# Optimization experiments

Measured on AMD Instinct MI355X. Metric: run time of the kernel, lower is better.

The kernel has to match this reference:

```python
import jax, jax.numpy as jnp
import numpy as np

B, H, S, D = 2, 16, 2048, 64
MASK_P = 0.1  # sparse random mask; avoids all-heads-masked NaN under softmax(dim=1)


def setup_inputs() -> dict:
    key = jax.random.key(0)
    kq, kk, kv, km = jax.random.split(key, 4)
    Q = jax.random.normal(kq, (B, H, S, D), dtype=jnp.float32)
    K = jax.random.normal(kk, (B, H, S, D), dtype=jnp.float32)
    V = jax.random.normal(kv, (B, H, S, D), dtype=jnp.float32)
    mask_bool = jax.random.uniform(km, (B, H, S, S)) < MASK_P
    return {"Q": Q, "K": K, "V": V, "mask_bool": mask_bool, "head_dim": D}


def reference(Q, K, V, mask_bool, head_dim):
    scale = jnp.sqrt(jnp.asarray(head_dim, dtype=Q.dtype))
    # scores: [B, H, Sq, Sk]
    scores = jnp.einsum("bhqd,bhkd->bhqk", Q, K) / scale
    scores = jnp.where(mask_bool, -jnp.inf, scores)
    # NOTE: source uses torch.softmax(..., dim=1) -> normalize over HEADS axis.
    attention_weight = jax.nn.softmax(scores, axis=1)
    # dropout module treated as identity (eval mode)
    context = jnp.einsum("bhqk,bhkd->bhqd", attention_weight, V)
    # transpose(1, 2) -> [B, Sq, H, D]
    return jnp.transpose(context, (0, 2, 1, 3))
```

## Files before the change

kernel.cpp:

```cpp
#include <hip/hip_runtime.h>
#include <stdint.h>
#include <math.h>

#define BB 2
#define HH 16
#define SS 2048
#define DD 64
#define QE  ((size_t)BB * HH * SS * DD)
#define PME ((size_t)BB * SS * SS)

typedef __attribute__((ext_vector_type(8))) short short8;
typedef __attribute__((ext_vector_type(4))) float float4v;

__device__ __forceinline__ float bflo(unsigned int u){ return __uint_as_float(u << 16); }
__device__ __forceinline__ float bfhi(unsigned int u){ return __uint_as_float(u & 0xffff0000u); }
__device__ __forceinline__ unsigned short f2bf(float f){
  unsigned int u = __float_as_uint(f);
  u += 0x7fffu + ((u >> 16) & 1u);
  return (unsigned short)(u >> 16);
}
__device__ __forceinline__ unsigned int pk2(float lo, float hi){
  return ((unsigned int)f2bf(hi) << 16) | (unsigned int)f2bf(lo);
}

__global__ void detect_mask_mode(const unsigned int* __restrict__ mw, int* __restrict__ mode_out){
  __shared__ int a32, af, a64;
  const int t = threadIdx.x;
  if (t == 0){ a32 = 1; af = 1; a64 = 1; }
  __syncthreads();
  int ok32 = 1, okf = 1, ok64 = 1;
  for (int idx = t; idx < 4096; idx += 256){
    const unsigned int w = mw[idx];
    if (w > 1u) ok32 = 0;
    if (w != 0u && w != 0x3F800000u) okf = 0;
    if ((idx & 1) ? (w != 0u) : (w > 1u)) ok64 = 0;
  }
  if (!ok32) atomicAnd(&a32, 0);
  if (!okf)  atomicAnd(&af, 0);
  if (!ok64) atomicAnd(&a64, 0);
  __syncthreads();
  if (t == 0){
    int mode;
    if (a64)      mode = 3;
    else if (a32) mode = 0;
    else if (af)  mode = 2;
    else          mode = 1;
    *mode_out = mode;
  }
}

__global__ __launch_bounds__(256) void pack_mask_kernel(
    const void* __restrict__ mask, const int* __restrict__ modep,
    unsigned short* __restrict__ pm)
{
  const int mode = *modep;
  const size_t tid  = (size_t)blockIdx.x * 256 + threadIdx.x;
  const size_t base = tid * 8;
  const size_t bq   = base >> 11;
  const int    k0   = (int)(base & (SS - 1));
  const size_t b    = bq >> 11;
  const size_t q    = bq & (SS - 1);

  unsigned short outv[8] = {0,0,0,0,0,0,0,0};

  if (mode == 0 || mode == 2){
    const unsigned int* p = (const unsigned int*)mask;
    #pragma unroll
    for (int h = 0; h < HH; ++h){
      const size_t e = ((b * HH + h) * SS + q) * SS + k0;
      const uint4 a = *(const uint4*)(p + e);
      const uint4 c = *(const uint4*)(p + e + 4);
      const unsigned short bit = (unsigned short)(1u << h);
      if (a.x) outv[0] |= bit;  if (a.y) outv[1] |= bit;
      if (a.z) outv[2] |= bit;  if (a.w) outv[3] |= bit;
      if (c.x) outv[4] |= bit;  if (c.y) outv[5] |= bit;
      if (c.z) outv[6] |= bit;  if (c.w) outv[7] |= bit;
    }
  } else if (mode == 1){
    const unsigned char* p = (const unsigned char*)mask;
    #pragma unroll
    for (int h = 0; h < HH; ++h){
      const size_t e = ((b * HH + h) * SS + q) * SS + k0;
      uint2 a = *(const uint2*)(p + e);
      const unsigned short bit = (unsigned short)(1u << h);
      #pragma unroll
      for (int j = 0; j < 4; ++j){
        if ((a.x >> (8*j)) & 0xffu) outv[j]     |= bit;
        if ((a.y >> (8*j)) & 0xffu) outv[4 + j] |= bit;
      }
    }
  } else {
    const unsigned int* p = (const unsigned int*)mask;
    #pragma unroll
    for (int h = 0; h < HH; ++h){
      const size_t e = (((b * HH + h) * SS + q) * SS + k0) * 2;
      const unsigned short bit = (unsigned short)(1u << h);
      #pragma unroll
      for (int j = 0; j < 4; ++j){
        const uint4 a = *(const uint4*)(p + e + j * 4);
        if (a.x) outv[j * 2]     |= bit;
        if (a.z) outv[j * 2 + 1] |= bit;
      }
    }
  }

  uint4 w;
  w.x = (unsigned int)outv[0] | ((unsigned int)outv[1] << 16);
  w.y = (unsigned int)outv[2] | ((unsigned int)outv[3] << 16);
  w.z = (unsigned int)outv[4] | ((unsigned int)outv[5] << 16);
  w.w = (unsigned int)outv[6] | ((unsigned int)outv[7] << 16);
  *(uint4*)(pm + base) = w;
}

__global__ void conv_bf16_kernel(const float* __restrict__ src, unsigned short* __restrict__ dst, float scale){
  const size_t i = ((size_t)blockIdx.x * 256 + threadIdx.x) * 8;
  const float4 a = *(const float4*)(src + i);
  const float4 b = *(const float4*)(src + i + 4);
  uint4 o;
  o.x = pk2(a.x * scale, a.y * scale);
  o.y = pk2(a.z * scale, a.w * scale);
  o.z = pk2(b.x * scale, b.y * scale);
  o.w = pk2(b.z * scale, b.w * scale);
  *(uint4*)(dst + i) = o;
}

__global__ void transp_v_kernel(const float* __restrict__ V, unsigned short* __restrict__ Vt){
  __shared__ unsigned short tile[64][66];
  const int t  = threadIdx.x;
  const int kt = blockIdx.x & 31;
  const int bh = blockIdx.x >> 5;
  {
    const int kr = t >> 2, dc = (t & 3) * 16;
    const float* src = V + ((size_t)bh * SS + (size_t)(kt * 64 + kr)) * DD + dc;
    #pragma unroll
    for (int c = 0; c < 4; ++c){
      const float4 v = *(const float4*)(src + c * 4);
      tile[kr][dc + c * 4 + 0] = f2bf(v.x);
      tile[kr][dc + c * 4 + 1] = f2bf(v.y);
      tile[kr][dc + c * 4 + 2] = f2bf(v.z);
      tile[kr][dc + c * 4 + 3] = f2bf(v.w);
    }
  }
  __syncthreads();
  {
    const int dr = t >> 2, kc = (t & 3) * 16;
    unsigned short* dst = Vt + ((size_t)bh * DD + dr) * SS + kt * 64 + kc;
    unsigned int w[8];
    #pragma unroll
    for (int p = 0; p < 8; ++p){
      w[p] = (unsigned int)tile[kc + 2*p][dr] | ((unsigned int)tile[kc + 2*p + 1][dr] << 16);
    }
    uint4 o0 = { w[0], w[1], w[2], w[3] };
    uint4 o1 = { w[4], w[5], w[6], w[7] };
    *(uint4*)(dst)     = o0;
    *(uint4*)(dst + 8) = o1;
  }
}

__global__ __launch_bounds__(256, 2) void attn_main_kernel(
    const unsigned short* __restrict__ Qb, const unsigned short* __restrict__ Kb,
    const unsigned short* __restrict__ Vt, const unsigned short* __restrict__ pm,
    float* __restrict__ out)
{
  __shared__ unsigned short Qf[HH * 2 * 512];
  __shared__ unsigned short W[HH * 16 * 64];

  const int t = threadIdx.x;
  const int wave = t >> 6, lane = t & 63, quad = lane >> 4, l16 = lane & 15;

  const int L  = blockIdx.x;
  const int b  = (L >> 1) & 1;
  const int kc = (L >> 2) & 1;
  const int q0 = (((L >> 3) << 1) | (L & 1)) * 16;

  float4v O[4][4];
  #pragma unroll
  for (int i = 0; i < 4; ++i)
    #pragma unroll
    for (int j = 0; j < 4; ++j) O[i][j] = (float4v){0.f, 0.f, 0.f, 0.f};

  #pragma unroll
  for (int hh = 0; hh < 4; ++hh){
    const int h = wave * 4 + hh;
    const unsigned short* qp = Qb + ((size_t)(b * HH + h) * SS + (size_t)(q0 + l16)) * DD + quad * 8;
    const short8 a0 = *(const short8*)(qp);
    const short8 a1 = *(const short8*)(qp + 32);
    *(short8*)&Qf[(h * 2 + 0) * 512 + lane * 8] = a0;
    *(short8*)&Qf[(h * 2 + 1) * 512 + lane * 8] = a1;
  }
  __syncthreads();

  #pragma unroll 1
  for (int ks = 0; ks < 16; ++ks){
    const int k0  = (kc * 16 + ks) * 64;
    const int k0w = k0 + wave * 16;

    const unsigned short* pmb = pm + ((size_t)b * SS + (size_t)(q0 + quad * 4)) * SS + (size_t)(k0w + l16);
    unsigned int m16[4];
    #pragma unroll
    for (int r = 0; r < 4; ++r) m16[r] = (unsigned int)pmb[(size_t)r * SS];

    unsigned int sp[HH][2];
    const unsigned short* kbase = Kb + ((size_t)(b * HH) * SS + (size_t)(k0w + l16)) * DD + quad * 8;

    #pragma unroll
    for (int ch = 0; ch < 2; ++ch){
      short8 kb0[8], kb1[8];
      #pragma unroll
      for (int j = 0; j < 8; ++j){
        const unsigned short* kp = kbase + (size_t)(ch * 8 + j) * (SS * DD);
        kb0[j] = *(const short8*)(kp);
        kb1[j] = *(const short8*)(kp + 32);
      }
      #pragma unroll
      for (int j = 0; j < 8; ++j){
        const int h = ch * 8 + j;
        const short8 a0 = *(const short8*)&Qf[(h * 2 + 0) * 512 + lane * 8];
        const short8 a1 = *(const short8*)&Qf[(h * 2 + 1) * 512 + lane * 8];
        float4v c = (float4v){0.f, 0.f, 0.f, 0.f};
        c = __builtin_amdgcn_mfma_f32_16x16x32_bf16(a0, kb0[j], c, 0, 0, 0);
        c = __builtin_amdgcn_mfma_f32_16x16x32_bf16(a1, kb1[j], c, 0, 0, 0);
        #pragma unroll
        for (int r = 0; r < 4; ++r) if ((m16[r] >> h) & 1u) c[r] = -INFINITY;
        sp[h][0] = pk2(c[0], c[1]);
        sp[h][1] = pk2(c[2], c[3]);
      }
    }

    #pragma unroll
    for (int r = 0; r < 4; ++r){
      const int row = quad * 4 + r;
      float sv[HH];
      float m = -INFINITY;
      #pragma unroll
      for (int h = 0; h < HH; ++h){
        const unsigned int u = sp[h][r >> 1];
        const float f = (r & 1) ? bfhi(u) : bflo(u);
        sv[h] = f;
        m = fmaxf(m, f);
      }
      float sum = 0.f;
      #pragma unroll
      for (int h = 0; h < HH; ++h){
        const float e = (sv[h] != -INFINITY) ? __expf(sv[h] - m) : 0.f;
        sv[h] = e;
        sum += e;
      }
      const float rinv = (sum > 0.f) ? (1.0f / sum) : 0.f;
      const int col = (wave * 16 + l16) ^ ((row & 7) << 3);
      #pragma unroll
      for (int h = 0; h < HH; ++h){
        W[h * 1024 + row * 64 + col] = f2bf(sv[h] * rinv);
      }
    }
    __syncthreads();

    {
      short8 aw[8];
      #pragma unroll
      for (int hh = 0; hh < 4; ++hh)
        #pragma unroll
        for (int kr = 0; kr < 2; ++kr){
          const int h = wave * 4 + hh;
          aw[hh * 2 + kr] = *(const short8*)&W[h * 1024 + l16 * 64 + ((kr * 32 + quad * 8) ^ ((l16 & 7) << 3))];
        }

      short8 vb[2][8];
      {
        const unsigned short* v0 = Vt + ((size_t)(b * HH + wave * 4) * DD + l16) * SS + k0 + quad * 8;
        #pragma unroll
        for (int kr = 0; kr < 2; ++kr)
          #pragma unroll
          for (int dt = 0; dt < 4; ++dt)
            vb[0][kr * 4 + dt] = *(const short8*)(v0 + (size_t)dt * 16 * SS + kr * 32);
      }
      #pragma unroll
      for (int hh = 0; hh < 4; ++hh){
        const int cur = hh & 1;
        if (hh < 3){
          const unsigned short* v1 = Vt + ((size_t)(b * HH + wave * 4 + hh + 1) * DD + l16) * SS + k0 + quad * 8;
          #pragma unroll
          for (int kr = 0; kr < 2; ++kr)
            #pragma unroll
            for (int dt = 0; dt < 4; ++dt)
              vb[cur ^ 1][kr * 4 + dt] = *(const short8*)(v1 + (size_t)dt * 16 * SS + kr * 32);
        }
        #pragma unroll
        for (int kr = 0; kr < 2; ++kr)
          #pragma unroll
          for (int dt = 0; dt < 4; ++dt)
            O[hh][dt] = __builtin_amdgcn_mfma_f32_16x16x32_bf16(aw[hh * 2 + kr], vb[cur][kr * 4 + dt], O[hh][dt], 0, 0, 0);
      }
    }
    __syncthreads();
  }

  #pragma unroll
  for (int hh = 0; hh < 4; ++hh){
    const int h = wave * 4 + hh;
    #pragma unroll
    for (int dt = 0; dt < 4; ++dt){
      #pragma unroll
      for (int r = 0; r < 4; ++r){
        float* op = out + (((size_t)b * SS + (size_t)(q0 + quad * 4 + r)) * HH + h) * DD + dt * 16 + l16;
        unsafeAtomicAdd(op, O[hh][dt][r]);
      }
    }
  }
}

extern "C" void kernel_launch(void* const* d_in, const int* in_sizes, int n_in,
                              void* d_out, int out_size, void* d_ws, size_t ws_size,
                              hipStream_t stream)
{
  const float* Q = (const float*)d_in[0];
  const float* K = (const float*)d_in[1];
  const float* V = (const float*)d_in[2];
  const void* mask = d_in[3];

  uintptr_t base = (uintptr_t)d_ws;
  int* mode_ptr       = (int*)base;
  unsigned short* Qb  = (unsigned short*)(base + 64);
  unsigned short* Kb  = Qb + QE;
  unsigned short* Vt  = Kb + QE;
  unsigned short* pmp = Vt + QE;

  detect_mask_mode<<<1, 256, 0, stream>>>((const unsigned int*)mask, mode_ptr);
  pack_mask_kernel<<<(int)(PME / (256 * 8)), 256, 0, stream>>>(mask, mode_ptr, pmp);
  conv_bf16_kernel<<<2048, 256, 0, stream>>>(Q, Qb, 0.125f);
  conv_bf16_kernel<<<2048, 256, 0, stream>>>(K, Kb, 1.0f);
  transp_v_kernel<<<BB * HH * (SS / 64), 256, 0, stream>>>(V, Vt);
  hipMemsetAsync(d_out, 0, (size_t)out_size * sizeof(float), stream);

  attn_main_kernel<<<512, 256, 0, stream>>>(Qb, Kb, Vt, pmp, (float*)d_out);
}
```

Measured before the change: 1.003 ms.

## Double-buffer softmax weights, drop trailing barrier, reload Q from global, prefetch mask

The softmax weight buffer in shared memory is now double-buffered by iteration parity, which lets the second barrier at the end of each key step be removed. Q fragments are no longer staged in shared memory and are re-read from global (likely cache-resident) memory in each chunk. The mask word for the next key step is prefetched after the QK MFMAs, and the launch-bounds occupancy hint is dropped. This cuts synchronisation and shared-memory traffic, at the cost of extra global Q loads and possibly higher register pressure without the occupancy hint.

Result: slower. 1.078 ms (+7.4%).

```diff
diff --git a/kernel.cpp b/kernel.cpp
--- a/kernel.cpp
+++ b/kernel.cpp
@@ -157,13 +157,12 @@
   }
 }
 
-__global__ __launch_bounds__(256, 2) void attn_main_kernel(
+__global__ __launch_bounds__(256) void attn_main_kernel(
     const unsigned short* __restrict__ Qb, const unsigned short* __restrict__ Kb,
     const unsigned short* __restrict__ Vt, const unsigned short* __restrict__ pm,
     float* __restrict__ out)
 {
-  __shared__ unsigned short Qf[HH * 2 * 512];
-  __shared__ unsigned short W[HH * 16 * 64];
+  __shared__ unsigned short W[2][HH * 16 * 64];
 
   const int t = threadIdx.x;
   const int wave = t >> 6, lane = t & 63, quad = lane >> 4, l16 = lane & 15;
@@ -179,47 +178,40 @@
     #pragma unroll
     for (int j = 0; j < 4; ++j) O[i][j] = (float4v){0.f, 0.f, 0.f, 0.f};
 
+  const unsigned short* qbase = Qb + ((size_t)(b * HH) * SS + (size_t)(q0 + l16)) * DD + quad * 8;
+  const unsigned short* kbas0 = Kb + ((size_t)(b * HH) * SS + (size_t)(kc * 1024 + wave * 16 + l16)) * DD + quad * 8;
+  const unsigned short* pmrow = pm + ((size_t)b * SS + (size_t)(q0 + quad * 4)) * SS + (size_t)(kc * 1024 + wave * 16 + l16);
+
+  unsigned int m16[4];
   #pragma unroll
-  for (int hh = 0; hh < 4; ++hh){
-    const int h = wave * 4 + hh;
-    const unsigned short* qp = Qb + ((size_t)(b * HH + h) * SS + (size_t)(q0 + l16)) * DD + quad * 8;
-    const short8 a0 = *(const short8*)(qp);
-    const short8 a1 = *(const short8*)(qp + 32);
-    *(short8*)&Qf[(h * 2 + 0) * 512 + lane * 8] = a0;
-    *(short8*)&Qf[(h * 2 + 1) * 512 + lane * 8] = a1;
-  }
-  __syncthreads();
+  for (int r = 0; r < 4; ++r) m16[r] = (unsigned int)pmrow[(size_t)r * SS];
 
   #pragma unroll 1
   for (int ks = 0; ks < 16; ++ks){
-    const int k0  = (kc * 16 + ks) * 64;
-    const int k0w = k0 + wave * 16;
-
-    const unsigned short* pmb = pm + ((size_t)b * SS + (size_t)(q0 + quad * 4)) * SS + (size_t)(k0w + l16);
-    unsigned int m16[4];
-    #pragma unroll
-    for (int r = 0; r < 4; ++r) m16[r] = (unsigned int)pmb[(size_t)r * SS];
+    const int k0 = (kc * 16 + ks) * 64;
 
     unsigned int sp[HH][2];
-    const unsigned short* kbase = Kb + ((size_t)(b * HH) * SS + (size_t)(k0w + l16)) * DD + quad * 8;
-
-    #pragma unroll
-    for (int ch = 0; ch < 2; ++ch){
-      short8 kb0[8], kb1[8];
-      #pragma unroll
-      for (int j = 0; j < 8; ++j){
-        const unsigned short* kp = kbase + (size_t)(ch * 8 + j) * (SS * DD);
+    const unsigned short* kbase = kbas0 + (size_t)ks * 64 * DD;
+
+    #pragma unroll
+    for (int ch = 0; ch < 4; ++ch){
+      short8 qa0[4], qa1[4], kb0[4], kb1[4];
+      #pragma unroll
+      for (int j = 0; j < 4; ++j){
+        const int h = ch * 4 + j;
+        const unsigned short* qp = qbase + (size_t)h * (SS * DD);
+        const unsigned short* kp = kbase + (size_t)h * (SS * DD);
+        qa0[j] = *(const short8*)(qp);
+        qa1[j] = *(const short8*)(qp + 32);
         kb0[j] = *(const short8*)(kp);
         kb1[j] = *(const short8*)(kp + 32);
       }
       #pragma unroll
-      for (int j = 0; j < 8; ++j){
-        const int h = ch * 8 + j;
-        const short8 a0 = *(const short8*)&Qf[(h * 2 + 0) * 512 + lane * 8];
-        const short8 a1 = *(const short8*)&Qf[(h * 2 + 1) * 512 + lane * 8];
+      for (int j = 0; j < 4; ++j){
+        const int h = ch * 4 + j;
         float4v c = (float4v){0.f, 0.f, 0.f, 0.f};
-        c = __builtin_amdgcn_mfma_f32_16x16x32_bf16(a0, kb0[j], c, 0, 0, 0);
-        c = __builtin_amdgcn_mfma_f32_16x16x32_bf16(a1, kb1[j], c, 0, 0, 0);
+        c = __builtin_amdgcn_mfma_f32_16x16x32_bf16(qa0[j], kb0[j], c, 0, 0, 0);
+        c = __builtin_amdgcn_mfma_f32_16x16x32_bf16(qa1[j], kb1[j], c, 0, 0, 0);
         #pragma unroll
         for (int r = 0; r < 4; ++r) if ((m16[r] >> h) & 1u) c[r] = -INFINITY;
         sp[h][0] = pk2(c[0], c[1]);
@@ -227,6 +219,12 @@
       }
     }
 
+    if (ks < 15){
+      #pragma unroll
+      for (int r = 0; r < 4; ++r) m16[r] = (unsigned int)pmrow[(size_t)r * SS + (size_t)(ks + 1) * 64];
+    }
+
+    unsigned short* Wc = &W[ks & 1][0];
     #pragma unroll
     for (int r = 0; r < 4; ++r){
       const int row = quad * 4 + r;
@@ -250,7 +248,7 @@
       const int col = (wave * 16 + l16) ^ ((row & 7) << 3);
       #pragma unroll
       for (int h = 0; h < HH; ++h){
-        W[h * 1024 + row * 64 + col] = f2bf(sv[h] * rinv);
+        Wc[h * 1024 + row * 64 + col] = f2bf(sv[h] * rinv);
       }
     }
     __syncthreads();
@@ -262,7 +260,7 @@
         #pragma unroll
         for (int kr = 0; kr < 2; ++kr){
           const int h = wave * 4 + hh;
-          aw[hh * 2 + kr] = *(const short8*)&W[h * 1024 + l16 * 64 + ((kr * 32 + quad * 8) ^ ((l16 & 7) << 3))];
+          aw[hh * 2 + kr] = *(const short8*)&Wc[h * 1024 + l16 * 64 + ((kr * 32 + quad * 8) ^ ((l16 & 7) << 3))];
         }
 
       short8 vb[2][8];
@@ -292,7 +290,6 @@
             O[hh][dt] = __builtin_amdgcn_mfma_f32_16x16x32_bf16(aw[hh * 2 + kr], vb[cur][kr * 4 + dt], O[hh][dt], 0, 0, 0);
       }
     }
-    __syncthreads();
   }
 
   #pragma unroll
```
